# Kernel optimization log

Measured on AMD Instinct MI355X. Metric: run time of the kernel, lower is better.

The kernel has to match this reference:

```python
import jax, jax.numpy as jnp
import numpy as np

N_NODES = 50000
N_EDGES = 640000
IN_DIM = 128
HID = 128
OUT_DIM = 16
BATCH = 2
EPS = 1e-5


def setup_inputs() -> dict:
    key = jax.random.key(0)
    ks = jax.random.split(key, 12)
    x = jax.random.normal(ks[0], (BATCH, N_NODES, IN_DIM), dtype=jnp.float32)
    edge_index = jax.random.randint(ks[1], (2, N_EDGES), 0, N_NODES, dtype=jnp.int32)
    # learned per-edge log-weights (initialized ~0 like nn.Parameter(zeros), small noise for a nontrivial test)
    edge_weight_param = 0.01 * jax.random.normal(ks[2], (N_EDGES,), dtype=jnp.float32)
    s1 = 1.0 / np.sqrt(IN_DIM)
    s2 = 1.0 / np.sqrt(HID)
    W1 = jax.random.uniform(ks[3], (IN_DIM, HID), minval=-s1, maxval=s1, dtype=jnp.float32)
    b1 = jnp.zeros((HID,), jnp.float32)
    W2 = jax.random.uniform(ks[4], (HID, HID), minval=-s2, maxval=s2, dtype=jnp.float32)
    b2 = jnp.zeros((HID,), jnp.float32)
    g1 = jnp.ones((HID,), jnp.float32); be1 = jnp.zeros((HID,), jnp.float32)
    g2 = jnp.ones((HID,), jnp.float32); be2 = jnp.zeros((HID,), jnp.float32)
    Wc = jax.random.uniform(ks[5], (HID, OUT_DIM), minval=-s2, maxval=s2, dtype=jnp.float32)
    bc = jax.random.uniform(ks[6], (OUT_DIM,), minval=-s2, maxval=s2, dtype=jnp.float32)
    return {"x": x, "edge_index": edge_index, "edge_weight_param": edge_weight_param,
            "W1": W1, "b1": b1, "W2": W2, "b2": b2,
            "g1": g1, "be1": be1, "g2": g2, "be2": be2,
            "Wc": Wc, "bc": bc}


def _gcn_norm(edge_index, edge_weight):
    # PyG GCNConv: add self-loops (weight 1), symmetric D^-1/2 A D^-1/2 normalization
    row = jnp.concatenate([edge_index[0], jnp.arange(N_NODES, dtype=edge_index.dtype)])
    col = jnp.concatenate([edge_index[1], jnp.arange(N_NODES, dtype=edge_index.dtype)])
    ew = jnp.concatenate([edge_weight, jnp.ones((N_NODES,), edge_weight.dtype)])
    deg = jax.ops.segment_sum(ew, col, num_segments=N_NODES)
    dinv = jnp.where(deg > 0, jax.lax.rsqrt(jnp.maximum(deg, 1e-30)), 0.0)
    norm = dinv[row] * ew * dinv[col]
    return row, col, norm


def _gcn_conv(x, W, b, row, col, norm):
    # x: [B, N, F_in] -> [B, N, F_out]; gather-scale-scatter over edges
    xw = x @ W                                   # [B, N, H]
    msg = xw[:, row, :] * norm[None, :, None]    # [B, E+N, H]
    out = jax.vmap(lambda m: jax.ops.segment_sum(m, col, num_segments=N_NODES))(msg)
    return out + b


def _batchnorm(h, gamma, beta):
    # training-mode BN over flattened (B*N) rows, biased variance, eps=1e-5
    B, N, F = h.shape
    hf = h.reshape(-1, F)
    mu = hf.mean(axis=0)
    var = hf.var(axis=0)
    return (((hf - mu) * jax.lax.rsqrt(var + EPS)) * gamma + beta).reshape(B, N, F)


def reference(x, edge_index, edge_weight_param, W1, b1, W2, b2, g1, be1, g2, be2, Wc, bc):
    edge_weight = jnp.exp(edge_weight_param)  # learned exp edge weights
    row, col, norm = _gcn_norm(edge_index, edge_weight)
    h = jax.nn.relu(_gcn_conv(x, W1, b1, row, col, norm))
    h = _batchnorm(h, g1, be1)
    # dropout is identity in eval / deterministic reference
    h = jax.nn.relu(_gcn_conv(h, W2, b2, row, col, norm))
    h = _batchnorm(h, g2, be2)
    return h @ Wc + bc  # [B, N, OUT_DIM]
```

## Files before the change

### kernel.cpp

```cpp
#include <hip/hip_runtime.h>
#include <hip/hip_bf16.h>
#include <cstdint>
#include <cstddef>

#define N_NODES 50000
#define N_EDGES 640000
#define ROWS    100000
#define HID     128
#define OUTD    16
#define AGG_BLOCKS 2048
#define MID_BLOCKS 32
#define SCAN_BLOCKS 196
#define GEMM_BLOCKS 512
#define GEMM_TILES  (ROWS / 16)
#define EG_BLOCKS   3500
#define EG_GEMM_WAVES 4000

typedef __attribute__((ext_vector_type(8))) uint16_t ushort8;
typedef __attribute__((ext_vector_type(8))) __bf16   bf16x8;
typedef __attribute__((ext_vector_type(4))) float    floatx4;

union FragU { ushort8 u; bf16x8 b; };

__device__ __forceinline__ float bf_lo(uint32_t u){
  union { uint32_t u; float f; } c; c.u = u << 16; return c.f;
}
__device__ __forceinline__ float bf_hi(uint32_t u){
  union { uint32_t u; float f; } c; c.u = u & 0xffff0000u; return c.f;
}
__device__ __forceinline__ uint16_t f2bf(float f){
  union { float f; uint32_t u; } c; c.f = f;
  uint32_t u = c.u;
  uint32_t r = (u + 0x7fffu + ((u >> 16) & 1u)) >> 16;
  return (uint16_t)r;
}

__device__ __forceinline__ void pack_w(int t, const float* __restrict__ W,
                                       const float* sca ,
                                       uint16_t* __restrict__ WP){
  int L = t & 63;
  int s = (t >> 6) & 3;
  int c = t >> 8;
  int n = (c >> 1) * 32 + 2 * (L & 15) + (c & 1);
  int k0 = s * 32 + (L >> 4) * 8;
  ushort8 r;
#pragma unroll
  for (int j = 0; j < 8; j++){
    float w = W[(size_t)(k0 + j) * HID + n];
    if (sca) w *= sca[k0 + j];
    r[j] = f2bf(w);
  }
  *((ushort8*)(WP + (size_t)t * 8)) = r;
}

__global__ void k_initpack(unsigned long long* __restrict__ dc,
                           const float* __restrict__ W1, uint16_t* __restrict__ WP1){
  int b = blockIdx.x;
  if (b < SCAN_BLOCKS){
    int i = b * 256 + threadIdx.x;
    if (i < N_NODES) dc[i] = 0ull;
  } else {
    pack_w((b - SCAN_BLOCKS) * 256 + threadIdx.x, W1, nullptr, WP1);
  }
}

__global__ __launch_bounds__(256, 2) void k_edge_gemm1(const int* __restrict__ ei,
                                                       const float* __restrict__ ewp,
                                                       unsigned long long* __restrict__ dc,
                                                       unsigned int* __restrict__ slot,
                                                       const float* __restrict__ X,
                                                       const uint16_t* __restrict__ WP,
                                                       uint16_t* __restrict__ Y){
  const int b = blockIdx.x;
  const int g = b % 7;
  if (g < 5){
    const int eb = (b / 7) * 5 + g;
    const int e = eb * 256 + threadIdx.x;
    float w = expf(ewp[e]);
    int c = ei[N_EDGES + e];
    unsigned long long inc = (1ull << 44) | (unsigned long long)(w * 1048576.0f + 0.5f);
    unsigned long long old = atomicAdd(&dc[c], inc);
    slot[e] = (unsigned int)(old >> 44);
    return;
  }
  const int lane = threadIdx.x & 63;
  const int wid  = threadIdx.x >> 6;
  const int gw   = ((b / 7) * 2 + (g - 5)) * 4 + wid;
  const int m    = lane & 15;
  const int kq   = lane >> 4;

  FragU wf[8][4];
#pragma unroll
  for (int c = 0; c < 8; c++)
#pragma unroll
    for (int s = 0; s < 4; s++)
      wf[c][s].u = *((const ushort8*)(WP + (size_t)(((c * 4 + s) * 64 + lane) * 8)));

  uint32_t* Yu = (uint32_t*)Y;
  for (int t = gw; t < GEMM_TILES; t += EG_GEMM_WAVES){
    const int row0 = t * 16;
    FragU af[4];
#pragma unroll
    for (int s = 0; s < 4; s++){
      const float* p = X + (size_t)(row0 + m) * HID + s * 32 + kq * 8;
      floatx4 f0 = *((const floatx4*)p);
      floatx4 f1 = *((const floatx4*)(p + 4));
      ushort8 r;
#pragma unroll
      for (int j = 0; j < 4; j++){ r[j] = f2bf(f0[j]); r[j + 4] = f2bf(f1[j]); }
      af[s].u = r;
    }
    floatx4 acc[8];
#pragma unroll
    for (int c = 0; c < 8; c++) acc[c] = floatx4{0.f, 0.f, 0.f, 0.f};
#pragma unroll
    for (int s = 0; s < 4; s++)
#pragma unroll
      for (int c = 0; c < 8; c++)
        acc[c] = __builtin_amdgcn_mfma_f32_16x16x32_bf16(af[s].b, wf[c][s].b, acc[c], 0, 0, 0);
#pragma unroll
    for (int t4 = 0; t4 < 4; t4++)
#pragma unroll
      for (int i = 0; i < 4; i++){
        uint32_t pr = (uint32_t)f2bf(acc[2 * t4][i]) | ((uint32_t)f2bf(acc[2 * t4 + 1][i]) << 16);
        Yu[(size_t)(row0 + kq * 4 + i) * 64 + t4 * 16 + m] = pr;
      }
  }
}

__global__ void k_scan_bsum(const unsigned long long* __restrict__ dc, int* __restrict__ bsum,
                            float* __restrict__ dinv){
  __shared__ int sd[256];
  int tid = threadIdx.x;
  int i = blockIdx.x * 256 + tid;
  int cnt = 0;
  if (i < N_NODES){
    unsigned long long v = dc[i];
    cnt = (int)(v >> 44);
    float deg = 1.0f + (float)((double)(v & ((1ull << 44) - 1)) * (1.0 / 1048576.0));
    dinv[i] = 1.0f / sqrtf(deg);
  }
  sd[tid] = cnt;
  __syncthreads();
  for (int off = 128; off > 0; off >>= 1){
    if (tid < off) sd[tid] += sd[tid + off];
    __syncthreads();
  }
  if (tid == 0) bsum[blockIdx.x] = sd[0];
}

__global__ void k_scan_write(const unsigned long long* __restrict__ dc, const int* __restrict__ bsum,
                             int* __restrict__ rp){
  __shared__ int sb[256];
  __shared__ int sd[256];
  int tid = threadIdx.x;
  sb[tid] = (tid < SCAN_BLOCKS && tid < blockIdx.x) ? bsum[tid] : 0;
  __syncthreads();
  for (int off = 128; off > 0; off >>= 1){
    if (tid < off) sb[tid] += sb[tid + off];
    __syncthreads();
  }
  const int base = sb[0];

  int i = blockIdx.x * 256 + tid;
  int v = (i < N_NODES) ? (int)(dc[i] >> 44) : 0;
  sd[tid] = v;
  __syncthreads();
  for (int off = 1; off < 256; off <<= 1){
    int t = (tid >= off) ? sd[tid - off] : 0;
    __syncthreads();
    sd[tid] += t;
    __syncthreads();
  }
  if (i < N_NODES) rp[i] = base + sd[tid] - v;
  if (blockIdx.x == 0 && tid == 0) rp[N_NODES] = N_EDGES;
}

__global__ void k_fill(const int* __restrict__ ei, const float* __restrict__ ewp,
                       const float* __restrict__ dinv, const unsigned int* __restrict__ slot,
                       const int* __restrict__ rp, unsigned long long* __restrict__ edg){
  int e = blockIdx.x * 256 + threadIdx.x;
  if (e < N_EDGES){
    int r = ei[e];
    int c = ei[N_EDGES + e];
    float w = expf(ewp[e]);
    float nrm = dinv[r] * w * dinv[c];
    int p = rp[c] + (int)slot[e];
    edg[p] = ((unsigned long long)__float_as_uint(nrm) << 32) | (unsigned int)r;
  }
}

__global__ __launch_bounds__(256, 2) void k_gemm2(const uint16_t* __restrict__ X,
                                                  const uint16_t* __restrict__ WP,
                                                  uint16_t* __restrict__ Y){
  const int lane = threadIdx.x & 63;
  const int wid  = threadIdx.x >> 6;
  const int gw   = blockIdx.x * 4 + wid;
  const int nw   = GEMM_BLOCKS * 4;
  const int m    = lane & 15;
  const int kq   = lane >> 4;

  FragU wf[8][4];
#pragma unroll
  for (int c = 0; c < 8; c++)
#pragma unroll
    for (int s = 0; s < 4; s++)
      wf[c][s].u = *((const ushort8*)(WP + (size_t)(((c * 4 + s) * 64 + lane) * 8)));

  uint32_t* Yu = (uint32_t*)Y;
  for (int t = gw; t < GEMM_TILES; t += nw){
    const int row0 = t * 16;
    FragU af[4];
#pragma unroll
    for (int s = 0; s < 4; s++)
      af[s].u = *((const ushort8*)(X + (size_t)(row0 + m) * HID + s * 32 + kq * 8));
    floatx4 acc[8];
#pragma unroll
    for (int c = 0; c < 8; c++) acc[c] = floatx4{0.f, 0.f, 0.f, 0.f};
#pragma unroll
    for (int s = 0; s < 4; s++)
#pragma unroll
      for (int c = 0; c < 8; c++)
        acc[c] = __builtin_amdgcn_mfma_f32_16x16x32_bf16(af[s].b, wf[c][s].b, acc[c], 0, 0, 0);
#pragma unroll
    for (int t4 = 0; t4 < 4; t4++)
#pragma unroll
      for (int i = 0; i < 4; i++){
        uint32_t pr = (uint32_t)f2bf(acc[2 * t4][i]) | ((uint32_t)f2bf(acc[2 * t4 + 1][i]) << 16);
        Yu[(size_t)(row0 + kq * 4 + i) * 64 + t4 * 16 + m] = pr;
      }
  }
}

__global__ __launch_bounds__(256) void k_cls_mfma(const uint16_t* __restrict__ H,
                                                  const uint16_t* __restrict__ WPC,
                                                  const float* __restrict__ cvec,
                                                  float* __restrict__ out){
  const int lane = threadIdx.x & 63;
  const int wid  = threadIdx.x >> 6;
  const int gw   = blockIdx.x * 4 + wid;
  const int nw   = GEMM_BLOCKS * 4;
  const int m    = lane & 15;
  const int kq   = lane >> 4;

  FragU wf[4];
#pragma unroll
  for (int s = 0; s < 4; s++)
    wf[s].u = *((const ushort8*)(WPC + (size_t)((s * 64 + lane) * 8)));
  const float cv = cvec[m];

  for (int t = gw; t < GEMM_TILES; t += nw){
    const int row0 = t * 16;
    FragU af[4];
#pragma unroll
    for (int s = 0; s < 4; s++)
      af[s].u = *((const ushort8*)(H + (size_t)(row0 + m) * HID + s * 32 + kq * 8));
    floatx4 acc = floatx4{0.f, 0.f, 0.f, 0.f};
#pragma unroll
    for (int s = 0; s < 4; s++)
      acc = __builtin_amdgcn_mfma_f32_16x16x32_bf16(af[s].b, wf[s].b, acc, 0, 0, 0);
#pragma unroll
    for (int i = 0; i < 4; i++)
      out[(size_t)(row0 + kq * 4 + i) * OUTD + m] = acc[i] + cv;
  }
}

__global__ __launch_bounds__(256) void k_agg(const uint16_t* __restrict__ XW,
                                             const int* __restrict__ rp,
                                             const unsigned long long* __restrict__ edg,
                                             const float* __restrict__ dinv,
                                             const float* __restrict__ bias,
                                             const float* __restrict__ cvec,
                                             uint16_t* __restrict__ H,
                                             float* __restrict__ psum,
                                             float* __restrict__ pssq){
  __shared__ float lsum[128];
  __shared__ float lssq[128];
  const int tid = threadIdx.x;
  if (tid < 128){ lsum[tid] = 0.f; lssq[tid] = 0.f; }
  __syncthreads();

  const int lane = tid & 63;
  const int wid  = tid >> 6;
  const int gw   = blockIdx.x * 4 + wid;
  const int nw   = AGG_BLOCKS * 4;
  const uint32_t* Xu = (const uint32_t*)XW;
  uint32_t* Hu = (uint32_t*)H;
  const int f0 = lane * 2;
  const float b0 = bias[f0], b1 = bias[f0 + 1];
  const float c0 = cvec ? cvec[f0] : 0.f;
  const float c1 = cvec ? cvec[f0 + 1] : 0.f;
  float ts0 = 0.f, ts1 = 0.f, tq0 = 0.f, tq1 = 0.f;

  int node = gw;
  if (node < N_NODES){
    int e0 = rp[node], e1 = rp[node + 1];
    float di = dinv[node];
    uint32_t s0 = Xu[(size_t)node * 64 + lane];
    uint32_t s1 = Xu[(size_t)(N_NODES + node) * 64 + lane];
    while (true){
      const int nn = node + nw;
      const bool more = (nn < N_NODES);
      int ne0 = 0, ne1 = 0; float ndi = 0.f; uint32_t ns0 = 0, ns1 = 0;
      if (more){
        ne0 = rp[nn]; ne1 = rp[nn + 1];
        ndi = dinv[nn];
        ns0 = Xu[(size_t)nn * 64 + lane];
        ns1 = Xu[(size_t)(N_NODES + nn) * 64 + lane];
      }

      const float sn = di * di;
      float a0x = sn * bf_lo(s0), a0y = sn * bf_hi(s0);
      float a1x = sn * bf_lo(s1), a1y = sn * bf_hi(s1);
      float wsum = sn;
      int e = e0;
      for (; e + 8 <= e1; e += 8){
        unsigned long long myrec = edg[e + (lane & 7)];
        uint32_t rlo = (uint32_t)myrec;
        uint32_t rhi = (uint32_t)(myrec >> 32);
        int srcs[8]; float ws[8];
#pragma unroll
        for (int u = 0; u < 8; u++){
          srcs[u] = __builtin_amdgcn_readlane(rlo, u);
          ws[u] = __uint_as_float((uint32_t)__builtin_amdgcn_readlane((int)rhi, u));
        }
        uint32_t q0[8], q1[8];
#pragma unroll
        for (int u = 0; u < 8; u++){
          q0[u] = Xu[(size_t)(uint32_t)srcs[u] * 64 + lane];
          q1[u] = Xu[(size_t)(N_NODES + (uint32_t)srcs[u]) * 64 + lane];
        }
#pragma unroll
        for (int u = 0; u < 8; u++){
          a0x = fmaf(ws[u], bf_lo(q0[u]), a0x); a0y = fmaf(ws[u], bf_hi(q0[u]), a0y);
          a1x = fmaf(ws[u], bf_lo(q1[u]), a1x); a1y = fmaf(ws[u], bf_hi(q1[u]), a1y);
          wsum += ws[u];
        }
      }
      for (; e + 4 <= e1; e += 4){
        unsigned long long myrec = edg[e + (lane & 3)];
        uint32_t rlo = (uint32_t)myrec;
        uint32_t rhi = (uint32_t)(myrec >> 32);
        int srcs[4]; float ws[4];
#pragma unroll
        for (int u = 0; u < 4; u++){
          srcs[u] = __builtin_amdgcn_readlane(rlo, u);
          ws[u] = __uint_as_float((uint32_t)__builtin_amdgcn_readlane((int)rhi, u));
        }
        uint32_t q0[4], q1[4];
#pragma unroll
        for (int u = 0; u < 4; u++){
          q0[u] = Xu[(size_t)(uint32_t)srcs[u] * 64 + lane];
          q1[u] = Xu[(size_t)(N_NODES + (uint32_t)srcs[u]) * 64 + lane];
        }
#pragma unroll
        for (int u = 0; u < 4; u++){
          a0x = fmaf(ws[u], bf_lo(q0[u]), a0x); a0y = fmaf(ws[u], bf_hi(q0[u]), a0y);
          a1x = fmaf(ws[u], bf_lo(q1[u]), a1x); a1y = fmaf(ws[u], bf_hi(q1[u]), a1y);
          wsum += ws[u];
        }
      }
      for (; e < e1; e++){
        unsigned long long rec = edg[e];
        size_t src = (uint32_t)rec;
        float w = __uint_as_float((uint32_t)(rec >> 32));
        uint32_t g0 = Xu[src * 64 + lane];
        uint32_t g1 = Xu[(N_NODES + src) * 64 + lane];
        a0x = fmaf(w, bf_lo(g0), a0x); a0y = fmaf(w, bf_hi(g0), a0y);
        a1x = fmaf(w, bf_lo(g1), a1x); a1y = fmaf(w, bf_hi(g1), a1y);
        wsum += w;
      }
      a0x = fmaxf(fmaf(wsum, c0, a0x) + b0, 0.f); a0y = fmaxf(fmaf(wsum, c1, a0y) + b1, 0.f);
      a1x = fmaxf(fmaf(wsum, c0, a1x) + b0, 0.f); a1y = fmaxf(fmaf(wsum, c1, a1y) + b1, 0.f);
      Hu[(size_t)node * 64 + lane]             = (uint32_t)f2bf(a0x) | ((uint32_t)f2bf(a0y) << 16);
      Hu[(size_t)(N_NODES + node) * 64 + lane] = (uint32_t)f2bf(a1x) | ((uint32_t)f2bf(a1y) << 16);
      ts0 += a0x + a1x; ts1 += a0y + a1y;
      tq0 += a0x * a0x + a1x * a1x; tq1 += a0y * a0y + a1y * a1y;

      if (!more) break;
      node = nn; e0 = ne0; e1 = ne1; di = ndi; s0 = ns0; s1 = ns1;
    }
  }

  atomicAdd(&lsum[f0],     ts0); atomicAdd(&lsum[f0 + 1], ts1);
  atomicAdd(&lssq[f0],     tq0); atomicAdd(&lssq[f0 + 1], tq1);
  __syncthreads();
  if (tid < 128){
    psum[(size_t)blockIdx.x * 128 + tid] = lsum[tid];
    pssq[(size_t)blockIdx.x * 128 + tid] = lssq[tid];
  }
}

__global__ __launch_bounds__(256) void k_bnmid(const float* __restrict__ psum,
                                               const float* __restrict__ pssq,
                                               float* __restrict__ msum,
                                               float* __restrict__ mssq){
  __shared__ float ss[2][128];
  __shared__ float sq[2][128];
  const int tid = threadIdx.x;
  const int f  = tid & 127;
  const int sl = tid >> 7;
  const int rows_per = AGG_BLOCKS / MID_BLOCKS;
  const int base = blockIdx.x * rows_per;
  float s = 0.f, q = 0.f;
  for (int r = base + sl; r < base + rows_per; r += 2){
    s += psum[(size_t)r * 128 + f];
    q += pssq[(size_t)r * 128 + f];
  }
  ss[sl][f] = s; sq[sl][f] = q;
  __syncthreads();
  if (tid < 128){
    msum[(size_t)blockIdx.x * 128 + tid] = ss[0][tid] + ss[1][tid];
    mssq[(size_t)blockIdx.x * 128 + tid] = sq[0][tid] + sq[1][tid];
  }
}

__device__ __forceinline__ void bn_finalize_lds(const float* __restrict__ msum,
                                                const float* __restrict__ mssq,
                                                const float* __restrict__ gamma,
                                                const float* __restrict__ beta,
                                                float* ssc, float* ssh){
  const int tid = threadIdx.x;
  if (tid < 128){
    float S = 0.f, Q = 0.f;
#pragma unroll
    for (int b = 0; b < MID_BLOCKS; b++){
      S += msum[(size_t)b * 128 + tid];
      Q += mssq[(size_t)b * 128 + tid];
    }
    const float inv = 1.0f / (float)ROWS;
    float mu = S * inv;
    float var = fmaxf(Q * inv - mu * mu, 0.f);
    float rstd = 1.0f / sqrtf(var + 1e-5f);
    float sc = gamma[tid] * rstd;
    ssc[tid] = sc;
    ssh[tid] = fmaf(-mu, sc, beta[tid]);
  }
  __syncthreads();
}

__global__ void k_prep2(const float* __restrict__ msum, const float* __restrict__ mssq,
                        const float* __restrict__ gamma, const float* __restrict__ beta,
                        const float* __restrict__ W2,
                        uint16_t* __restrict__ WP2, float* __restrict__ C2){
  __shared__ float ssc[128];
  __shared__ float ssh[128];
  bn_finalize_lds(msum, mssq, gamma, beta, ssc, ssh);
  if (blockIdx.x < 8){
    pack_w(blockIdx.x * 256 + threadIdx.x, W2, ssc, WP2);
  } else if (threadIdx.x < 128){
    const int j = threadIdx.x;
    float a = 0.f;
    for (int k = 0; k < HID; k++) a = fmaf(ssh[k], W2[(size_t)k * HID + j], a);
    C2[j] = a;
  }
}

__global__ void k_prepc(const float* __restrict__ msum, const float* __restrict__ mssq,
                        const float* __restrict__ gamma, const float* __restrict__ beta,
                        const float* __restrict__ Wc, const float* __restrict__ bc,
                        uint16_t* __restrict__ WPC, float* __restrict__ CVC){
  __shared__ float ssc[128];
  __shared__ float ssh[128];
  bn_finalize_lds(msum, mssq, gamma, beta, ssc, ssh);
  if (blockIdx.x == 0){
    int t = threadIdx.x;
    int L = t & 63;
    int s = t >> 6;
    int n = L & 15;
    int k0 = s * 32 + (L >> 4) * 8;
    ushort8 r;
#pragma unroll
    for (int j = 0; j < 8; j++)
      r[j] = f2bf(ssc[k0 + j] * Wc[(size_t)(k0 + j) * OUTD + n]);
    *((ushort8*)(WPC + (size_t)t * 8)) = r;
  } else if (threadIdx.x < OUTD){
    const int j = threadIdx.x;
    float a = bc[j];
    for (int k = 0; k < HID; k++) a = fmaf(ssh[k], Wc[(size_t)k * OUTD + j], a);
    CVC[j] = a;
  }
}

extern "C" void kernel_launch(void* const* d_in, const int* in_sizes, int n_in,
                              void* d_out, int out_size, void* d_ws, size_t ws_size,
                              hipStream_t stream){
  const float* x   = (const float*)d_in[0];
  const int*   ei  = (const int*)d_in[1];
  const float* ewp = (const float*)d_in[2];
  const float* W1  = (const float*)d_in[3];
  const float* b1  = (const float*)d_in[4];
  const float* W2  = (const float*)d_in[5];
  const float* b2  = (const float*)d_in[6];
  const float* g1  = (const float*)d_in[7];
  const float* be1 = (const float*)d_in[8];
  const float* g2  = (const float*)d_in[9];
  const float* be2 = (const float*)d_in[10];
  const float* Wc  = (const float*)d_in[11];
  const float* bc  = (const float*)d_in[12];
  float* out = (float*)d_out;

  char* wsb = (char*)d_ws;
  size_t off = 0;
  auto give = [&](size_t bytes) -> void* {
    void* p = wsb + off;
    off = (off + bytes + 255) & ~(size_t)255;
    return p;
  };
  uint16_t* XW  = (uint16_t*)give((size_t)ROWS * 128 * 2);
  uint16_t* Hb  = (uint16_t*)give((size_t)ROWS * 128 * 2);
  unsigned long long* DC  = (unsigned long long*)give((size_t)N_NODES * 8);
  unsigned long long* EDG = (unsigned long long*)give((size_t)N_EDGES * 8);
  unsigned int* SLOT = (unsigned int*)give((size_t)N_EDGES * 4);
  float* DINV   = (float*)give((size_t)N_NODES * 4);
  int*   RP     = (int*)give((size_t)(N_NODES + 1) * 4);
  int*   BSUM   = (int*)give(1024);
  float* PSUM   = (float*)give((size_t)AGG_BLOCKS * 128 * 4);
  float* PSSQ   = (float*)give((size_t)AGG_BLOCKS * 128 * 4);
  float* MSUM   = (float*)give((size_t)MID_BLOCKS * 128 * 4);
  float* MSSQ   = (float*)give((size_t)MID_BLOCKS * 128 * 4);
  uint16_t* WP1 = (uint16_t*)give((size_t)HID * HID * 2);
  uint16_t* WP2 = (uint16_t*)give((size_t)HID * HID * 2);
  uint16_t* WPC = (uint16_t*)give((size_t)HID * OUTD * 2);
  float* C2     = (float*)give(512);
  float* CVC    = (float*)give(64);
  (void)ws_size; (void)n_in; (void)in_sizes; (void)out_size;

  k_initpack<<<SCAN_BLOCKS + 8, 256, 0, stream>>>(DC, W1, WP1);
  k_edge_gemm1<<<EG_BLOCKS, 256, 0, stream>>>(ei, ewp, DC, SLOT, x, WP1, XW);
  k_scan_bsum<<<SCAN_BLOCKS, 256, 0, stream>>>(DC, BSUM, DINV);
  k_scan_write<<<SCAN_BLOCKS, 256, 0, stream>>>(DC, BSUM, RP);
  k_fill<<<(N_EDGES + 255) / 256, 256, 0, stream>>>(ei, ewp, DINV, SLOT, RP, EDG);
  k_agg<<<AGG_BLOCKS, 256, 0, stream>>>(XW, RP, EDG, DINV, b1, nullptr, Hb, PSUM, PSSQ);
  k_bnmid<<<MID_BLOCKS, 256, 0, stream>>>(PSUM, PSSQ, MSUM, MSSQ);
  k_prep2<<<9, 256, 0, stream>>>(MSUM, MSSQ, g1, be1, W2, WP2, C2);
  k_gemm2<<<GEMM_BLOCKS, 256, 0, stream>>>(Hb, WP2, XW);
  k_agg<<<AGG_BLOCKS, 256, 0, stream>>>(XW, RP, EDG, DINV, b2, C2, Hb, PSUM, PSSQ);
  k_bnmid<<<MID_BLOCKS, 256, 0, stream>>>(PSUM, PSSQ, MSUM, MSSQ);
  k_prepc<<<2, 256, 0, stream>>>(MSUM, MSSQ, g2, be2, Wc, bc, WPC, CVC);
  k_cls_mfma<<<GEMM_BLOCKS, 256, 0, stream>>>(Hb, WPC, CVC, out);
}
```

Measured before the change: 314.5 us.

## Interleave batch XW rows per node and prefetch edge records in aggregation

The GEMM kernels now write XW in a node-major layout that interleaves the two batch rows, so each node's features for both batches sit in one 256-element row. The aggregation kernel then fetches both batches with one 64-bit load per lane instead of two scattered 32-bit loads. The edge loop is unified into 8-wide chunks with a partial tail, and the next chunk's edge records (including the next node's first chunk) are prefetched one iteration ahead. This cuts gather transactions and hides edge-record latency, at the cost of more complex control flow and clamped redundant loads.

```diff
diff --git a/kernel.cpp b/kernel.cpp
--- a/kernel.cpp
+++ b/kernel.cpp
@@ -99,6 +99,8 @@
   uint32_t* Yu = (uint32_t*)Y;
   for (int t = gw; t < GEMM_TILES; t += EG_GEMM_WAVES){
     const int row0 = t * 16;
+    const int bsel = (row0 >= N_NODES) ? 1 : 0;
+    const int nb = row0 - bsel * N_NODES;
     FragU af[4];
 #pragma unroll
     for (int s = 0; s < 4; s++){
@@ -123,7 +125,7 @@
 #pragma unroll
       for (int i = 0; i < 4; i++){
         uint32_t pr = (uint32_t)f2bf(acc[2 * t4][i]) | ((uint32_t)f2bf(acc[2 * t4 + 1][i]) << 16);
-        Yu[(size_t)(row0 + kq * 4 + i) * 64 + t4 * 16 + m] = pr;
+        Yu[(size_t)(nb + kq * 4 + i) * 128 + (t4 * 16 + m) * 2 + bsel] = pr;
       }
   }
 }
@@ -210,6 +212,8 @@
   uint32_t* Yu = (uint32_t*)Y;
   for (int t = gw; t < GEMM_TILES; t += nw){
     const int row0 = t * 16;
+    const int bsel = (row0 >= N_NODES) ? 1 : 0;
+    const int nb = row0 - bsel * N_NODES;
     FragU af[4];
 #pragma unroll
     for (int s = 0; s < 4; s++)
@@ -227,7 +231,7 @@
 #pragma unroll
       for (int i = 0; i < 4; i++){
         uint32_t pr = (uint32_t)f2bf(acc[2 * t4][i]) | ((uint32_t)f2bf(acc[2 * t4 + 1][i]) << 16);
-        Yu[(size_t)(row0 + kq * 4 + i) * 64 + t4 * 16 + m] = pr;
+        Yu[(size_t)(nb + kq * 4 + i) * 128 + (t4 * 16 + m) * 2 + bsel] = pr;
       }
   }
 }
@@ -284,92 +288,84 @@
   const int wid  = tid >> 6;
   const int gw   = blockIdx.x * 4 + wid;
   const int nw   = AGG_BLOCKS * 4;
-  const uint32_t* Xu = (const uint32_t*)XW;
+  const unsigned long long* Xq = (const unsigned long long*)XW;
   uint32_t* Hu = (uint32_t*)H;
   const int f0 = lane * 2;
   const float b0 = bias[f0], b1 = bias[f0 + 1];
   const float c0 = cvec ? cvec[f0] : 0.f;
   const float c1 = cvec ? cvec[f0 + 1] : 0.f;
   float ts0 = 0.f, ts1 = 0.f, tq0 = 0.f, tq1 = 0.f;
+  const int lu = lane & 7;
 
   int node = gw;
   if (node < N_NODES){
     int e0 = rp[node], e1 = rp[node + 1];
     float di = dinv[node];
-    uint32_t s0 = Xu[(size_t)node * 64 + lane];
-    uint32_t s1 = Xu[(size_t)(N_NODES + node) * 64 + lane];
+    unsigned long long sv = Xq[(size_t)node * 64 + lane];
+    unsigned long long rec = 0ull;
+    if (e0 < e1){
+      int a = e0 + lu; if (a > N_EDGES - 1) a = N_EDGES - 1;
+      rec = edg[a];
+    }
     while (true){
       const int nn = node + nw;
       const bool more = (nn < N_NODES);
-      int ne0 = 0, ne1 = 0; float ndi = 0.f; uint32_t ns0 = 0, ns1 = 0;
+      int ne0 = 0, ne1 = 0; float ndi = 0.f; unsigned long long nsv = 0ull;
       if (more){
         ne0 = rp[nn]; ne1 = rp[nn + 1];
         ndi = dinv[nn];
-        ns0 = Xu[(size_t)nn * 64 + lane];
-        ns1 = Xu[(size_t)(N_NODES + nn) * 64 + lane];
+        nsv = Xq[(size_t)nn * 64 + lane];
       }
 
       const float sn = di * di;
+      const uint32_t s0 = (uint32_t)sv, s1 = (uint32_t)(sv >> 32);
       float a0x = sn * bf_lo(s0), a0y = sn * bf_hi(s0);
       float a1x = sn * bf_lo(s1), a1y = sn * bf_hi(s1);
       float wsum = sn;
-      int e = e0;
-      for (; e + 8 <= e1; e += 8){
-        unsigned long long myrec = edg[e + (lane & 7)];
-        uint32_t rlo = (uint32_t)myrec;
-        uint32_t rhi = (uint32_t)(myrec >> 32);
-        int srcs[8]; float ws[8];
-#pragma unroll
-        for (int u = 0; u < 8; u++){
-          srcs[u] = __builtin_amdgcn_readlane(rlo, u);
-          ws[u] = __uint_as_float((uint32_t)__builtin_amdgcn_readlane((int)rhi, u));
+
+      for (int e = e0; e < e1; e += 8){
+        const int r = e1 - e;
+        const uint32_t rlo = (uint32_t)rec;
+        const uint32_t rhi = (uint32_t)(rec >> 32);
+        const int pe = (r > 8) ? (e + 8) : (more ? ne0 : -1);
+        if (pe >= 0){
+          int a = pe + lu; if (a > N_EDGES - 1) a = N_EDGES - 1;
+          rec = edg[a];
         }
-        uint32_t q0[8], q1[8];
-#pragma unroll
-        for (int u = 0; u < 8; u++){
-          q0[u] = Xu[(size_t)(uint32_t)srcs[u] * 64 + lane];
-          q1[u] = Xu[(size_t)(N_NODES + (uint32_t)srcs[u]) * 64 + lane];
-        }
-#pragma unroll
-        for (int u = 0; u < 8; u++){
-          a0x = fmaf(ws[u], bf_lo(q0[u]), a0x); a0y = fmaf(ws[u], bf_hi(q0[u]), a0y);
-          a1x = fmaf(ws[u], bf_lo(q1[u]), a1x); a1y = fmaf(ws[u], bf_hi(q1[u]), a1y);
-          wsum += ws[u];
+        unsigned long long q[8];
+        if (r >= 8){
+#pragma unroll
+          for (int u = 0; u < 8; u++)
+            q[u] = Xq[(size_t)(uint32_t)__builtin_amdgcn_readlane((int)rlo, u) * 64 + lane];
+#pragma unroll
+          for (int u = 0; u < 8; u++){
+            const float w = __uint_as_float((uint32_t)__builtin_amdgcn_readlane((int)rhi, u));
+            const uint32_t g0 = (uint32_t)q[u], g1 = (uint32_t)(q[u] >> 32);
+            a0x = fmaf(w, bf_lo(g0), a0x); a0y = fmaf(w, bf_hi(g0), a0y);
+            a1x = fmaf(w, bf_lo(g1), a1x); a1y = fmaf(w, bf_hi(g1), a1y);
+            wsum += w;
+          }
+        } else {
+#pragma unroll
+          for (int u = 0; u < 8; u++)
+            if (u < r)
+              q[u] = Xq[(size_t)(uint32_t)__builtin_amdgcn_readlane((int)rlo, u) * 64 + lane];
+#pragma unroll
+          for (int u = 0; u < 8; u++)
+            if (u < r){
+              const float w = __uint_as_float((uint32_t)__builtin_amdgcn_readlane((int)rhi, u));
+              const uint32_t g0 = (uint32_t)q[u], g1 = (uint32_t)(q[u] >> 32);
+              a0x = fmaf(w, bf_lo(g0), a0x); a0y = fmaf(w, bf_hi(g0), a0y);
+              a1x = fmaf(w, bf_lo(g1), a1x); a1y = fmaf(w, bf_hi(g1), a1y);
+              wsum += w;
+            }
         }
       }
-      for (; e + 4 <= e1; e += 4){
-        unsigned long long myrec = edg[e + (lane & 3)];
-        uint32_t rlo = (uint32_t)myrec;
-        uint32_t rhi = (uint32_t)(myrec >> 32);
-        int srcs[4]; float ws[4];
-#pragma unroll
-        for (int u = 0; u < 4; u++){
-          srcs[u] = __builtin_amdgcn_readlane(rlo, u);
-          ws[u] = __uint_as_float((uint32_t)__builtin_amdgcn_readlane((int)rhi, u));
-        }
-        uint32_t q0[4], q1[4];
-#pragma unroll
-        for (int u = 0; u < 4; u++){
-          q0[u] = Xu[(size_t)(uint32_t)srcs[u] * 64 + lane];
-          q1[u] = Xu[(size_t)(N_NODES + (uint32_t)srcs[u]) * 64 + lane];
-        }
-#pragma unroll
-        for (int u = 0; u < 4; u++){
-          a0x = fmaf(ws[u], bf_lo(q0[u]), a0x); a0y = fmaf(ws[u], bf_hi(q0[u]), a0y);
-          a1x = fmaf(ws[u], bf_lo(q1[u]), a1x); a1y = fmaf(ws[u], bf_hi(q1[u]), a1y);
-          wsum += ws[u];
-        }
+      if (e0 == e1 && more){
+        int a = ne0 + lu; if (a > N_EDGES - 1) a = N_EDGES - 1;
+        rec = edg[a];
       }
-      for (; e < e1; e++){
-        unsigned long long rec = edg[e];
-        size_t src = (uint32_t)rec;
-        float w = __uint_as_float((uint32_t)(rec >> 32));
-        uint32_t g0 = Xu[src * 64 + lane];
-        uint32_t g1 = Xu[(N_NODES + src) * 64 + lane];
-        a0x = fmaf(w, bf_lo(g0), a0x); a0y = fmaf(w, bf_hi(g0), a0y);
-        a1x = fmaf(w, bf_lo(g1), a1x); a1y = fmaf(w, bf_hi(g1), a1y);
-        wsum += w;
-      }
+
       a0x = fmaxf(fmaf(wsum, c0, a0x) + b0, 0.f); a0y = fmaxf(fmaf(wsum, c1, a0y) + b1, 0.f);
       a1x = fmaxf(fmaf(wsum, c0, a1x) + b0, 0.f); a1y = fmaxf(fmaf(wsum, c1, a1y) + b1, 0.f);
       Hu[(size_t)node * 64 + lane]             = (uint32_t)f2bf(a0x) | ((uint32_t)f2bf(a0y) << 16);
@@ -378,7 +374,7 @@
       tq0 += a0x * a0x + a1x * a1x; tq1 += a0y * a0y + a1y * a1y;
 
       if (!more) break;
-      node = nn; e0 = ne0; e1 = ne1; di = ndi; s0 = ns0; s1 = ns1;
+      node = nn; e0 = ne0; e1 = ne1; di = ndi; sv = nsv;
     }
   }
 
```

After: 323.3 us. 1.03x slower.
